# Performance work log

Measured on AMD Instinct MI355X. Metric: run time of the kernel, lower is better.

## Reference

```python
import jax, jax.numpy as jnp
import numpy as np

B, T, S, D = 8, 2048, 2048, 1024

def setup_inputs() -> dict:
    key = jax.random.key(0)
    k1, k2 = jax.random.split(key)
    trg_outs = jax.random.normal(k1, (B, T, D), dtype=jnp.float32)
    src_outs = jax.random.normal(k2, (B, S, D), dtype=jnp.float32)
    return {"trg_outs": trg_outs, "src_outs": src_outs}

def reference(trg_outs, src_outs):
    # Luong 'dot' attention: unscaled dot-product scores.
    # scores: (B, T, S)
    attn_scores = jnp.einsum('btd,bsd->bts', trg_outs, src_outs)
    attn_weights = jax.nn.softmax(attn_scores, axis=2)
    # context: (B, T, D)
    context_vec = jnp.einsum('bts,bsd->btd', attn_weights, src_outs)
    return (context_vec, attn_weights)
```

## Files before the change

### kernel.cpp

```cpp
#include <hip/hip_runtime.h>


#define BB 8
#define TT 2048
#define SS 2048
#define DD 1024

typedef float  f32x4   __attribute__((ext_vector_type(4)));
typedef float  f32x16  __attribute__((ext_vector_type(16)));
typedef short  bf16x8  __attribute__((ext_vector_type(8)));
typedef _Float16 f16x8 __attribute__((ext_vector_type(8)));
typedef _Float16 f16x4 __attribute__((ext_vector_type(4)));

static __device__ __forceinline__ unsigned short bf16_rne(float x) {
  unsigned int u = __float_as_uint(x);
  u += 0x7FFFu + ((u >> 16) & 1u);
  return (unsigned short)(u >> 16);
}

static __device__ __forceinline__ void gl2lds16(const void* g, void* l) {
  __builtin_amdgcn_global_load_lds(
      (const __attribute__((address_space(1))) unsigned int*)g,
      (__attribute__((address_space(3))) unsigned int*)l, 16, 0, 0);
}

static __device__ __forceinline__ int ldsoff_h(int r, int h) {
  return ((r >> 2) << 6) + ((((r & 3) << 1) + (h ^ ((r >> 2) & 1))) << 3);
}

__global__ __launch_bounds__(256)
void conv_trg_f16(const float* __restrict__ x, _Float16* __restrict__ h16) {
  const size_t i = ((size_t)blockIdx.x * 256 + threadIdx.x) * 8;
  float4 v0 = *(const float4*)(x + i);
  float4 v1 = *(const float4*)(x + i + 4);
  f16x8 h;
  h[0] = (_Float16)v0.x; h[1] = (_Float16)v0.y;
  h[2] = (_Float16)v0.z; h[3] = (_Float16)v0.w;
  h[4] = (_Float16)v1.x; h[5] = (_Float16)v1.y;
  h[6] = (_Float16)v1.z; h[7] = (_Float16)v1.w;
  *(f16x8*)(h16 + i) = h;
}

__global__ __launch_bounds__(256)
void conv_src_f16_hilo_t(const float* __restrict__ src,
                         _Float16* __restrict__ hi,
                         _Float16* __restrict__ lo,
                         _Float16* __restrict__ srcT) {
  const int b  = blockIdx.z;
  const int d0 = blockIdx.x * 64;
  const int s0 = blockIdx.y * 64;
  const float* S = src + (size_t)b * SS * DD;
  __shared__ _Float16 t16[64][65];
  const int t = threadIdx.x;

#pragma unroll
  for (int p = 0; p < 4; ++p) {
    const int r = p * 16 + (t >> 4);
    const int c = (t & 15) * 4;
    float4 v = *(const float4*)(S + (size_t)(s0 + r) * DD + d0 + c);
    float f[4] = {v.x, v.y, v.z, v.w};
    f16x4 h, l;
#pragma unroll
    for (int e = 0; e < 4; ++e) {
      _Float16 hv = (_Float16)f[e];
      h[e] = hv;
      l[e] = (_Float16)(f[e] - (float)hv);
      t16[r][c + e] = hv;
    }
    const size_t go = ((size_t)b * SS + s0 + r) * DD + d0 + c;
    *(f16x4*)(hi + go) = h;
    *(f16x4*)(lo + go) = l;
  }
  __syncthreads();
#pragma unroll
  for (int p = 0; p < 4; ++p) {
    const int d  = p * 16 + (t >> 4);
    const int sq = (t & 15) * 4;
    f16x4 o;
#pragma unroll
    for (int k = 0; k < 4; ++k) o[k] = t16[sq + k][d];
    *(f16x4*)(srcT + ((size_t)b * DD + d0 + d) * SS + s0 + sq) = o;
  }
}

__global__ __launch_bounds__(512, 2)
void attn_gemm1_pipe(const _Float16* __restrict__ a16,
                     const _Float16* __restrict__ bh16,
                     const _Float16* __restrict__ bl16,
                     float* __restrict__ scores) {
  const int b   = blockIdx.z;
  const int tm0 = blockIdx.y * 256;
  const int tn0 = blockIdx.x * 256;
  float* C = scores + (size_t)b * TT * SS;

  __shared__ __align__(16) _Float16 sm[3][24576];

  const int t      = threadIdx.x;
  const int lane   = t & 63;
  const int wv     = t >> 6;
  const int wm     = (wv >> 2) * 128;
  const int wn     = (wv & 3) * 64;
  const int lrow32 = lane & 31;
  const int khalf  = lane >> 5;

  const _Float16* gp[6];
  {
    const _Float16* base0 = a16  + ((size_t)b * TT + tm0) * DD;
    const _Float16* base1 = bh16 + ((size_t)b * SS + tn0) * DD;
    const _Float16* base2 = bl16 + ((size_t)b * SS + tn0) * DD;
    const _Float16* bases[3] = {base0, base1, base2};
#pragma unroll
    for (int j = 0; j < 6; ++j) {
      const int kk   = j & 1;
      const int cc   = t;
      const int line = cc >> 3, slot = cc & 7;
      const int r    = (line << 2) + (slot >> 1);
      const int h    = (slot & 1) ^ (line & 1);
      gp[j] = bases[j >> 1] + (size_t)r * DD + kk * 16 + h * 8;
    }
  }
#define STG1(buf, j) do { gl2lds16(gp[j], (buf) + ((j) * 512 + t) * 8); gp[j] += 32; } while (0)

  int aoff[4], bhoff[2], bloff[2];
#pragma unroll
  for (int mi = 0; mi < 4; ++mi)
    aoff[mi] = ldsoff_h(wm + mi * 32 + lrow32, khalf);
#pragma unroll
  for (int ni = 0; ni < 2; ++ni) {
    const int rr = wn + ni * 32 + lrow32;
    bhoff[ni] = 8192  + ldsoff_h(rr, khalf);
    bloff[ni] = 16384 + ldsoff_h(rr, khalf);
  }

  f32x16 acc[4][2];
#pragma unroll
  for (int i = 0; i < 4; ++i)
#pragma unroll
    for (int j = 0; j < 2; ++j) acc[i][j] = (f32x16)0.0f;

  _Float16* bufc = sm[0];
  _Float16* bufo = sm[1];
  _Float16* bufn = sm[2];

#pragma unroll
  for (int j = 0; j < 6; ++j) STG1(bufc, j);
#pragma unroll
  for (int j = 0; j < 6; ++j) STG1(bufo, j);
  asm volatile("s_waitcnt vmcnt(6)" ::: "memory");
  __builtin_amdgcn_s_barrier();
  __builtin_amdgcn_sched_barrier(0);

  const int NT = DD / 32;
#pragma unroll 1
  for (int tt = 0; tt < NT; ++tt) {
    const bool more = (tt + 2 < NT);

    {
      f16x8 a[4], bh[2], bl[2];
#pragma unroll
      for (int mi = 0; mi < 4; ++mi) a[mi] = *(const f16x8*)(bufc + aoff[mi]);
#pragma unroll
      for (int ni = 0; ni < 2; ++ni) {
        bh[ni] = *(const f16x8*)(bufc + bhoff[ni]);
        bl[ni] = *(const f16x8*)(bufc + bloff[ni]);
      }
      if (more) { STG1(bufn, 0); STG1(bufn, 1); STG1(bufn, 2); }
      __builtin_amdgcn_s_barrier();
      asm volatile("s_waitcnt lgkmcnt(0)" ::: "memory");
      __builtin_amdgcn_sched_barrier(0);
      __builtin_amdgcn_s_setprio(1);
#pragma unroll
      for (int mi = 0; mi < 4; ++mi)
#pragma unroll
        for (int ni = 0; ni < 2; ++ni) {
          acc[mi][ni] = __builtin_amdgcn_mfma_f32_32x32x16_f16(a[mi], bh[ni], acc[mi][ni], 0, 0, 0);
          acc[mi][ni] = __builtin_amdgcn_mfma_f32_32x32x16_f16(a[mi], bl[ni], acc[mi][ni], 0, 0, 0);
        }
      __builtin_amdgcn_s_setprio(0);
      __builtin_amdgcn_s_barrier();
      __builtin_amdgcn_sched_barrier(0);
    }

    {
      f16x8 a[4], bh[2], bl[2];
#pragma unroll
      for (int mi = 0; mi < 4; ++mi) a[mi] = *(const f16x8*)(bufc + 4096 + aoff[mi]);
#pragma unroll
      for (int ni = 0; ni < 2; ++ni) {
        bh[ni] = *(const f16x8*)(bufc + 4096 + bhoff[ni]);
        bl[ni] = *(const f16x8*)(bufc + 4096 + bloff[ni]);
      }
      if (more) { STG1(bufn, 3); STG1(bufn, 4); STG1(bufn, 5); }
      if (more) asm volatile("s_waitcnt vmcnt(6)" ::: "memory");
      else      asm volatile("s_waitcnt vmcnt(0)" ::: "memory");
      __builtin_amdgcn_s_barrier();
      asm volatile("s_waitcnt lgkmcnt(0)" ::: "memory");
      __builtin_amdgcn_sched_barrier(0);
      __builtin_amdgcn_s_setprio(1);
#pragma unroll
      for (int mi = 0; mi < 4; ++mi)
#pragma unroll
        for (int ni = 0; ni < 2; ++ni) {
          acc[mi][ni] = __builtin_amdgcn_mfma_f32_32x32x16_f16(a[mi], bh[ni], acc[mi][ni], 0, 0, 0);
          acc[mi][ni] = __builtin_amdgcn_mfma_f32_32x32x16_f16(a[mi], bl[ni], acc[mi][ni], 0, 0, 0);
        }
      __builtin_amdgcn_s_setprio(0);
      __builtin_amdgcn_s_barrier();
      __builtin_amdgcn_sched_barrier(0);
    }

    _Float16* tmp = bufc; bufc = bufo; bufo = bufn; bufn = tmp;
  }
#undef STG1

  const int rsub = 4 * khalf;
#pragma unroll
  for (int mi = 0; mi < 4; ++mi)
#pragma unroll
    for (int ni = 0; ni < 2; ++ni) {
      const int rb  = tm0 + wm + mi * 32 + rsub;
      const int col = tn0 + wn + ni * 32 + lrow32;
#pragma unroll
      for (int p = 0; p < 16; ++p)
        C[(size_t)(rb + (p & 3) + 8 * (p >> 2)) * SS + col] = acc[mi][ni][p];
    }
}

__global__ __launch_bounds__(64)
void attn_softmax_w16(float* __restrict__ w, _Float16* __restrict__ w16) {
  const size_t row = blockIdx.x;
  float4* p4 = (float4*)(w + row * SS);
  _Float16* o = w16 + row * SS;
  const int lane = threadIdx.x;

  float4 v[8];
#pragma unroll
  for (int j = 0; j < 8; ++j) v[j] = p4[lane + 64 * j];

  float m = -1e30f;
#pragma unroll
  for (int j = 0; j < 8; ++j)
    m = fmaxf(m, fmaxf(fmaxf(v[j].x, v[j].y), fmaxf(v[j].z, v[j].w)));
#pragma unroll
  for (int off = 32; off >= 1; off >>= 1) m = fmaxf(m, __shfl_xor(m, off, 64));

  float s = 0.0f;
#pragma unroll
  for (int j = 0; j < 8; ++j) {
    v[j].x = __expf(v[j].x - m); v[j].y = __expf(v[j].y - m);
    v[j].z = __expf(v[j].z - m); v[j].w = __expf(v[j].w - m);
    s += v[j].x + v[j].y + v[j].z + v[j].w;
  }
#pragma unroll
  for (int off = 32; off >= 1; off >>= 1) s += __shfl_xor(s, off, 64);

  const float inv = __fdividef(1.0f, s);
#pragma unroll
  for (int j = 0; j < 8; ++j) {
    v[j].x *= inv; v[j].y *= inv; v[j].z *= inv; v[j].w *= inv;
    p4[lane + 64 * j] = v[j];
    f16x4 h;
    h[0] = (_Float16)v[j].x; h[1] = (_Float16)v[j].y;
    h[2] = (_Float16)v[j].z; h[3] = (_Float16)v[j].w;
    *(f16x4*)(o + 4 * (lane + 64 * j)) = h;
  }
}

__global__ __launch_bounds__(512, 2)
void attn_gemm2_pipe(const _Float16* __restrict__ w16,
                     const _Float16* __restrict__ srcT,
                     float* __restrict__ out) {
  const int b   = blockIdx.z;
  const int tm0 = blockIdx.y * 256;
  const int tn0 = blockIdx.x * 256;
  float* C = out + (size_t)b * TT * DD;

  __shared__ __align__(16) _Float16 sm[3][16384];

  const int t      = threadIdx.x;
  const int lane   = t & 63;
  const int wv     = t >> 6;
  const int wm     = (wv >> 2) * 128;
  const int wn     = (wv & 3) * 64;
  const int lrow32 = lane & 31;
  const int khalf  = lane >> 5;

  const _Float16* gp[4];
  {
    const _Float16* base0 = w16  + ((size_t)b * TT + tm0) * SS;
    const _Float16* base1 = srcT + ((size_t)b * DD + tn0) * SS;
    const _Float16* bases[2] = {base0, base1};
#pragma unroll
    for (int j = 0; j < 4; ++j) {
      const int kk   = j & 1;
      const int cc   = t;
      const int line = cc >> 3, slot = cc & 7;
      const int r    = (line << 2) + (slot >> 1);
      const int h    = (slot & 1) ^ (line & 1);
      gp[j] = bases[j >> 1] + (size_t)r * SS + kk * 16 + h * 8;
    }
  }
#define STG2(buf, j) do { gl2lds16(gp[j], (buf) + ((j) * 512 + t) * 8); gp[j] += 32; } while (0)

  int aoff[4], boff[2];
#pragma unroll
  for (int mi = 0; mi < 4; ++mi)
    aoff[mi] = ldsoff_h(wm + mi * 32 + lrow32, khalf);
#pragma unroll
  for (int ni = 0; ni < 2; ++ni)
    boff[ni] = 8192 + ldsoff_h(wn + ni * 32 + lrow32, khalf);

  f32x16 acc[4][2];
#pragma unroll
  for (int i = 0; i < 4; ++i)
#pragma unroll
    for (int j = 0; j < 2; ++j) acc[i][j] = (f32x16)0.0f;

  _Float16* bufc = sm[0];
  _Float16* bufo = sm[1];
  _Float16* bufn = sm[2];

#pragma unroll
  for (int j = 0; j < 4; ++j) STG2(bufc, j);
#pragma unroll
  for (int j = 0; j < 4; ++j) STG2(bufo, j);
  asm volatile("s_waitcnt vmcnt(4)" ::: "memory");
  __builtin_amdgcn_s_barrier();
  __builtin_amdgcn_sched_barrier(0);

  const int NT = SS / 32;
#pragma unroll 1
  for (int tt = 0; tt < NT; ++tt) {
    const bool more = (tt + 2 < NT);

    {
      f16x8 a[4], bf[2];
#pragma unroll
      for (int mi = 0; mi < 4; ++mi) a[mi] = *(const f16x8*)(bufc + aoff[mi]);
#pragma unroll
      for (int ni = 0; ni < 2; ++ni) bf[ni] = *(const f16x8*)(bufc + boff[ni]);
      if (more) { STG2(bufn, 0); STG2(bufn, 2); }
      __builtin_amdgcn_s_barrier();
      asm volatile("s_waitcnt lgkmcnt(0)" ::: "memory");
      __builtin_amdgcn_sched_barrier(0);
      __builtin_amdgcn_s_setprio(1);
#pragma unroll
      for (int mi = 0; mi < 4; ++mi)
#pragma unroll
        for (int ni = 0; ni < 2; ++ni)
          acc[mi][ni] = __builtin_amdgcn_mfma_f32_32x32x16_f16(a[mi], bf[ni], acc[mi][ni], 0, 0, 0);
      __builtin_amdgcn_s_setprio(0);
      __builtin_amdgcn_s_barrier();
      __builtin_amdgcn_sched_barrier(0);
    }

    {
      f16x8 a[4], bf[2];
#pragma unroll
      for (int mi = 0; mi < 4; ++mi) a[mi] = *(const f16x8*)(bufc + 4096 + aoff[mi]);
#pragma unroll
      for (int ni = 0; ni < 2; ++ni) bf[ni] = *(const f16x8*)(bufc + 4096 + boff[ni]);
      if (more) { STG2(bufn, 1); STG2(bufn, 3); }
      if (more) asm volatile("s_waitcnt vmcnt(4)" ::: "memory");
      else      asm volatile("s_waitcnt vmcnt(0)" ::: "memory");
      __builtin_amdgcn_s_barrier();
      asm volatile("s_waitcnt lgkmcnt(0)" ::: "memory");
      __builtin_amdgcn_sched_barrier(0);
      __builtin_amdgcn_s_setprio(1);
#pragma unroll
      for (int mi = 0; mi < 4; ++mi)
#pragma unroll
        for (int ni = 0; ni < 2; ++ni)
          acc[mi][ni] = __builtin_amdgcn_mfma_f32_32x32x16_f16(a[mi], bf[ni], acc[mi][ni], 0, 0, 0);
      __builtin_amdgcn_s_setprio(0);
      __builtin_amdgcn_s_barrier();
      __builtin_amdgcn_sched_barrier(0);
    }

    _Float16* tmp = bufc; bufc = bufo; bufo = bufn; bufn = tmp;
  }
#undef STG2

  const int rsub = 4 * khalf;
#pragma unroll
  for (int mi = 0; mi < 4; ++mi)
#pragma unroll
    for (int ni = 0; ni < 2; ++ni) {
      const int rb  = tm0 + wm + mi * 32 + rsub;
      const int col = tn0 + wn + ni * 32 + lrow32;
#pragma unroll
      for (int p = 0; p < 16; ++p)
        C[(size_t)(rb + (p & 3) + 8 * (p >> 2)) * DD + col] = acc[mi][ni][p];
    }
}

__global__ __launch_bounds__(256, 1)
void attn_gemm1_scores_bf16x3(const float* __restrict__ trg,
                              const float* __restrict__ src,
                              float* __restrict__ scores) {
  const int b   = blockIdx.z;
  const int tm0 = blockIdx.y * 128;
  const int tn0 = blockIdx.x * 128;
  const float* A  = trg + (size_t)b * TT * DD;
  const float* Bm = src + (size_t)b * SS * DD;
  float* C = scores + (size_t)b * TT * SS;

  __shared__ __align__(16) unsigned short smAh[128 * 32];
  __shared__ __align__(16) unsigned short smAl[128 * 32];
  __shared__ __align__(16) unsigned short smBh[128 * 32];
  __shared__ __align__(16) unsigned short smBl[128 * 32];

  const int t     = threadIdx.x;
  const int lane  = t & 63;
  const int wv    = t >> 6;
  const int m_off = (wv & 1) * 64;
  const int n_off = (wv >> 1) * 64;
  const int q     = lane >> 4;
  const int lrow  = lane & 15;

  f32x4 acc[4][4];
#pragma unroll
  for (int i = 0; i < 4; ++i)
#pragma unroll
    for (int j = 0; j < 4; ++j) acc[i][j] = (f32x4)0.0f;

  for (int kt = 0; kt < DD; kt += 32) {
    __syncthreads();
#pragma unroll
    for (int h = 0; h < 2; ++h) {
      const int c  = t + h * 256;
      const int r  = c >> 2;
      const int j  = c & 3;
      const int gk = j ^ ((r >> 1) & 3);
      {
        const float* ga = A + (size_t)(tm0 + r) * DD + kt + gk * 8;
        float4 v0 = *(const float4*)ga;
        float4 v1 = *(const float4*)(ga + 4);
        float f[8] = {v0.x, v0.y, v0.z, v0.w, v1.x, v1.y, v1.z, v1.w};
        bf16x8 hi, lo;
#pragma unroll
        for (int e = 0; e < 8; ++e) {
          unsigned short hb = bf16_rne(f[e]);
          hi[e] = (short)hb;
          float hf = __uint_as_float(((unsigned int)hb) << 16);
          lo[e] = (short)bf16_rne(f[e] - hf);
        }
        *(bf16x8*)(smAh + c * 8) = hi;
        *(bf16x8*)(smAl + c * 8) = lo;
      }
      {
        const float* gb = Bm + (size_t)(tn0 + r) * DD + kt + gk * 8;
        float4 v0 = *(const float4*)gb;
        float4 v1 = *(const float4*)(gb + 4);
        float f[8] = {v0.x, v0.y, v0.z, v0.w, v1.x, v1.y, v1.z, v1.w};
        bf16x8 hi, lo;
#pragma unroll
        for (int e = 0; e < 8; ++e) {
          unsigned short hb = bf16_rne(f[e]);
          hi[e] = (short)hb;
          float hf = __uint_as_float(((unsigned int)hb) << 16);
          lo[e] = (short)bf16_rne(f[e] - hf);
        }
        *(bf16x8*)(smBh + c * 8) = hi;
        *(bf16x8*)(smBl + c * 8) = lo;
      }
    }
    __syncthreads();

    bf16x8 ah[4], al[4], bh[4], bl[4];
#pragma unroll
    for (int mi = 0; mi < 4; ++mi) {
      const int r   = m_off + mi * 16 + lrow;
      const int off = (r * 4 + (q ^ ((r >> 1) & 3))) * 8;
      ah[mi] = *(const bf16x8*)(smAh + off);
      al[mi] = *(const bf16x8*)(smAl + off);
    }
#pragma unroll
    for (int ni = 0; ni < 4; ++ni) {
      const int r   = n_off + ni * 16 + lrow;
      const int off = (r * 4 + (q ^ ((r >> 1) & 3))) * 8;
      bh[ni] = *(const bf16x8*)(smBh + off);
      bl[ni] = *(const bf16x8*)(smBl + off);
    }
#pragma unroll
    for (int mi = 0; mi < 4; ++mi)
#pragma unroll
      for (int ni = 0; ni < 4; ++ni) {
        acc[mi][ni] = __builtin_amdgcn_mfma_f32_16x16x32_bf16(al[mi], bh[ni], acc[mi][ni], 0, 0, 0);
        acc[mi][ni] = __builtin_amdgcn_mfma_f32_16x16x32_bf16(ah[mi], bl[ni], acc[mi][ni], 0, 0, 0);
        acc[mi][ni] = __builtin_amdgcn_mfma_f32_16x16x32_bf16(ah[mi], bh[ni], acc[mi][ni], 0, 0, 0);
      }
  }

#pragma unroll
  for (int mi = 0; mi < 4; ++mi)
#pragma unroll
    for (int ni = 0; ni < 4; ++ni) {
      const int row0 = tm0 + m_off + mi * 16 + q * 4;
      const int col  = tn0 + n_off + ni * 16 + lrow;
#pragma unroll
      for (int p = 0; p < 4; ++p)
        C[(size_t)(row0 + p) * SS + col] = acc[mi][ni][p];
    }
}

__global__ __launch_bounds__(256)
void attn_softmax_rows(float* __restrict__ w) {
  float* p = w + (size_t)blockIdx.x * SS;
  const int t = threadIdx.x;
  float4* p4 = (float4*)p;
  float4 v0 = p4[t];
  float4 v1 = p4[t + 256];

  float m = fmaxf(fmaxf(fmaxf(v0.x, v0.y), fmaxf(v0.z, v0.w)),
                  fmaxf(fmaxf(v1.x, v1.y), fmaxf(v1.z, v1.w)));
#pragma unroll
  for (int off = 32; off >= 1; off >>= 1) m = fmaxf(m, __shfl_xor(m, off, 64));
  __shared__ float redm[4];
  __shared__ float reds[4];
  const int wv = t >> 6, lane = t & 63;
  if (lane == 0) redm[wv] = m;
  __syncthreads();
  m = fmaxf(fmaxf(redm[0], redm[1]), fmaxf(redm[2], redm[3]));

  v0.x = __expf(v0.x - m); v0.y = __expf(v0.y - m);
  v0.z = __expf(v0.z - m); v0.w = __expf(v0.w - m);
  v1.x = __expf(v1.x - m); v1.y = __expf(v1.y - m);
  v1.z = __expf(v1.z - m); v1.w = __expf(v1.w - m);

  float s = v0.x + v0.y + v0.z + v0.w + v1.x + v1.y + v1.z + v1.w;
#pragma unroll
  for (int off = 32; off >= 1; off >>= 1) s += __shfl_xor(s, off, 64);
  if (lane == 0) reds[wv] = s;
  __syncthreads();
  s = reds[0] + reds[1] + reds[2] + reds[3];

  const float inv = __fdividef(1.0f, s);
  v0.x *= inv; v0.y *= inv; v0.z *= inv; v0.w *= inv;
  v1.x *= inv; v1.y *= inv; v1.z *= inv; v1.w *= inv;
  p4[t] = v0;
  p4[t + 256] = v1;
}

__global__ __launch_bounds__(256, 1)
void attn_gemm2_ctx_f16(const float* __restrict__ w,
                        const float* __restrict__ src,
                        float* __restrict__ out) {
  const int b   = blockIdx.z;
  const int tm0 = blockIdx.y * 128;
  const int tn0 = blockIdx.x * 128;
  const float* A  = w + (size_t)b * TT * SS;
  const float* Bs = src + (size_t)b * SS * DD;
  float* C = out + (size_t)b * TT * DD;

  __shared__ __align__(16) _Float16 smA[128 * 32];
  __shared__ __align__(16) _Float16 smB[128 * 32];

  const int t     = threadIdx.x;
  const int lane  = t & 63;
  const int wv    = t >> 6;
  const int m_off = (wv & 1) * 64;
  const int n_off = (wv >> 1) * 64;
  const int q     = lane >> 4;
  const int lrow  = lane & 15;

  const int bn    = t & 127;
  const int bh2   = t >> 7;
  const int bs2   = (bn >> 1) & 3;
  const int slot0 = (2 * bh2) ^ bs2;
  const int slot1 = (2 * bh2 + 1) ^ bs2;

  f32x4 acc[4][4];
#pragma unroll
  for (int i = 0; i < 4; ++i)
#pragma unroll
    for (int j = 0; j < 4; ++j) acc[i][j] = (f32x4)0.0f;

  for (int kt = 0; kt < SS; kt += 32) {
    __syncthreads();
#pragma unroll
    for (int h = 0; h < 2; ++h) {
      const int c  = t + h * 256;
      const int r  = c >> 2;
      const int j  = c & 3;
      const int gk = j ^ ((r >> 1) & 3);
      const float* ga = A + (size_t)(tm0 + r) * SS + kt + gk * 8;
      float4 v0 = *(const float4*)ga;
      float4 v1 = *(const float4*)(ga + 4);
      f16x8 hv;
      hv[0] = (_Float16)v0.x; hv[1] = (_Float16)v0.y;
      hv[2] = (_Float16)v0.z; hv[3] = (_Float16)v0.w;
      hv[4] = (_Float16)v1.x; hv[5] = (_Float16)v1.y;
      hv[6] = (_Float16)v1.z; hv[7] = (_Float16)v1.w;
      *(f16x8*)(smA + c * 8) = hv;
    }
    {
      const float* gb = Bs + (size_t)(kt + bh2 * 16) * DD + (tn0 + bn);
      f16x8 c0, c1;
#pragma unroll
      for (int kk = 0; kk < 8; ++kk) c0[kk] = (_Float16)gb[(size_t)kk * DD];
#pragma unroll
      for (int kk = 0; kk < 8; ++kk) c1[kk] = (_Float16)gb[(size_t)(kk + 8) * DD];
      *(f16x8*)(smB + bn * 32 + slot0 * 8) = c0;
      *(f16x8*)(smB + bn * 32 + slot1 * 8) = c1;
    }
    __syncthreads();

    f16x8 af[4], bfr[4];
#pragma unroll
    for (int mi = 0; mi < 4; ++mi) {
      const int r   = m_off + mi * 16 + lrow;
      const int off = (r * 4 + (q ^ ((r >> 1) & 3))) * 8;
      af[mi] = *(const f16x8*)(smA + off);
    }
#pragma unroll
    for (int ni = 0; ni < 4; ++ni) {
      const int n   = n_off + ni * 16 + lrow;
      const int off = n * 32 + (q ^ ((n >> 1) & 3)) * 8;
      bfr[ni] = *(const f16x8*)(smB + off);
    }
#pragma unroll
    for (int mi = 0; mi < 4; ++mi)
#pragma unroll
      for (int ni = 0; ni < 4; ++ni)
        acc[mi][ni] = __builtin_amdgcn_mfma_f32_16x16x32_f16(af[mi], bfr[ni], acc[mi][ni], 0, 0, 0);
  }

#pragma unroll
  for (int mi = 0; mi < 4; ++mi)
#pragma unroll
    for (int ni = 0; ni < 4; ++ni) {
      const int row0 = tm0 + m_off + mi * 16 + q * 4;
      const int col  = tn0 + n_off + ni * 16 + lrow;
#pragma unroll
      for (int p = 0; p < 4; ++p)
        C[(size_t)(row0 + p) * DD + col] = acc[mi][ni][p];
    }
}

extern "C" void kernel_launch(void* const* d_in, const int* in_sizes, int n_in,
                              void* d_out, int out_size, void* d_ws, size_t ws_size,
                              hipStream_t stream) {
  const float* trg = (const float*)d_in[0];
  const float* src = (const float*)d_in[1];
  float* ctx = (float*)d_out;
  float* wts = (float*)d_out + (size_t)BB * TT * DD;

  const size_t NT = (size_t)BB * TT * DD;
  const size_t NW = (size_t)BB * TT * SS;
  const size_t need = (4 * NT + NW) * 2;

  if (ws_size >= need) {
    _Float16* tH16 = (_Float16*)d_ws;
    _Float16* sH16 = tH16 + NT;
    _Float16* sL16 = sH16 + NT;
    _Float16* srcT = sL16 + NT;
    _Float16* w16  = srcT + NT;

    conv_trg_f16<<<dim3(NT / (8 * 256)), 256, 0, stream>>>(trg, tH16);
    conv_src_f16_hilo_t<<<dim3(DD / 64, SS / 64, BB), 256, 0, stream>>>(src, sH16, sL16, srcT);
    attn_gemm1_pipe<<<dim3(SS / 256, TT / 256, BB), 512, 0, stream>>>(tH16, sH16, sL16, wts);
    attn_softmax_w16<<<dim3(BB * TT), 64, 0, stream>>>(wts, w16);
    attn_gemm2_pipe<<<dim3(DD / 256, TT / 256, BB), 512, 0, stream>>>(w16, srcT, ctx);
  } else {
    attn_gemm1_scores_bf16x3<<<dim3(SS / 128, TT / 128, BB), 256, 0, stream>>>(trg, src, wts);
    attn_softmax_rows<<<dim3(BB * TT), 256, 0, stream>>>(wts);
    attn_gemm2_ctx_f16<<<dim3(DD / 128, TT / 128, BB), 256, 0, stream>>>(wts, src, ctx);
  }
}
```

Before: 575.5 us.

## Fuse fp32-to-fp16 weight conversion into second GEMM, drop fp16 weight buffer

The softmax kernel no longer writes a separate fp16 copy of the attention weights. The second GEMM now loads fp32 weights into registers, converts them to fp16 and stores them into LDS, while srcT is still staged directly into LDS. This removes a 64MB fp16 write and re-read, but the GEMM now reads fp32 weights (twice the bytes) once per DD/256 column block. It also replaces the 3-buffer direct-to-LDS pipeline with 2-buffer software prefetch through registers, which adds register pressure.

```diff
diff --git a/kernel.cpp b/kernel.cpp
--- a/kernel.cpp
+++ b/kernel.cpp
@@ -227,10 +227,9 @@
 }
 
 __global__ __launch_bounds__(64)
-void attn_softmax_w16(float* __restrict__ w, _Float16* __restrict__ w16) {
+void attn_softmax_inplace(float* __restrict__ w) {
   const size_t row = blockIdx.x;
   float4* p4 = (float4*)(w + row * SS);
-  _Float16* o = w16 + row * SS;
   const int lane = threadIdx.x;
 
   float4 v[8];
@@ -259,23 +258,21 @@
   for (int j = 0; j < 8; ++j) {
     v[j].x *= inv; v[j].y *= inv; v[j].z *= inv; v[j].w *= inv;
     p4[lane + 64 * j] = v[j];
-    f16x4 h;
-    h[0] = (_Float16)v[j].x; h[1] = (_Float16)v[j].y;
-    h[2] = (_Float16)v[j].z; h[3] = (_Float16)v[j].w;
-    *(f16x4*)(o + 4 * (lane + 64 * j)) = h;
   }
 }
 
 __global__ __launch_bounds__(512, 2)
-void attn_gemm2_pipe(const _Float16* __restrict__ w16,
-                     const _Float16* __restrict__ srcT,
-                     float* __restrict__ out) {
+void attn_g2_fused(const float* __restrict__ w,
+                   const _Float16* __restrict__ srcT,
+                   float* __restrict__ out) {
   const int b   = blockIdx.z;
+  const int tn0 = blockIdx.x * 256;
   const int tm0 = blockIdx.y * 256;
-  const int tn0 = blockIdx.x * 256;
+  const float* W = w + (size_t)b * TT * SS;
   float* C = out + (size_t)b * TT * DD;
 
-  __shared__ __align__(16) _Float16 sm[3][16384];
+  __shared__ __align__(16) _Float16 smA[2][8192];
+  __shared__ __align__(16) _Float16 smB[2][8192];
 
   const int t      = threadIdx.x;
   const int lane   = t & 63;
@@ -285,22 +282,24 @@
   const int lrow32 = lane & 31;
   const int khalf  = lane >> 5;
 
-  const _Float16* gp[4];
-  {
-    const _Float16* base0 = w16  + ((size_t)b * TT + tm0) * SS;
-    const _Float16* base1 = srcT + ((size_t)b * DD + tn0) * SS;
-    const _Float16* bases[2] = {base0, base1};
-#pragma unroll
-    for (int j = 0; j < 4; ++j) {
-      const int kk   = j & 1;
-      const int cc   = t;
-      const int line = cc >> 3, slot = cc & 7;
-      const int r    = (line << 2) + (slot >> 1);
-      const int h    = (slot & 1) ^ (line & 1);
-      gp[j] = bases[j >> 1] + (size_t)r * SS + kk * 16 + h * 8;
-    }
-  }
-#define STG2(buf, j) do { gl2lds16(gp[j], (buf) + ((j) * 512 + t) * 8); gp[j] += 32; } while (0)
+  const float* gw[4];
+  int wadr[4];
+#pragma unroll
+  for (int p = 0; p < 4; ++p) {
+    const int c    = p * 512 + t;
+    const int rloc = c >> 3;
+    const int f4   = c & 7;
+    const int kk   = f4 >> 2;
+    const int h    = (f4 >> 1) & 1;
+    const int sub  = f4 & 1;
+    wadr[p] = kk * 4096 + ldsoff_h(rloc, h) + sub * 4;
+    gw[p] = W + (size_t)(tm0 + rloc) * SS + f4 * 4;
+  }
+
+  const int ar = (t >> 3) * 4 + ((t & 7) >> 1);
+  const int ah = ((t & 7) & 1) ^ ((t >> 3) & 1);
+  const _Float16* gpB0 = srcT + ((size_t)b * DD + tn0 + ar) * SS + ah * 8;
+  const _Float16* gpB1 = gpB0 + 16;
 
   int aoff[4], boff[2];
 #pragma unroll
@@ -308,7 +307,7 @@
     aoff[mi] = ldsoff_h(wm + mi * 32 + lrow32, khalf);
 #pragma unroll
   for (int ni = 0; ni < 2; ++ni)
-    boff[ni] = 8192 + ldsoff_h(wn + ni * 32 + lrow32, khalf);
+    boff[ni] = ldsoff_h(wn + ni * 32 + lrow32, khalf);
 
   f32x16 acc[4][2];
 #pragma unroll
@@ -316,70 +315,105 @@
 #pragma unroll
     for (int j = 0; j < 2; ++j) acc[i][j] = (f32x16)0.0f;
 
-  _Float16* bufc = sm[0];
-  _Float16* bufo = sm[1];
-  _Float16* bufn = sm[2];
-
-#pragma unroll
-  for (int j = 0; j < 4; ++j) STG2(bufc, j);
-#pragma unroll
-  for (int j = 0; j < 4; ++j) STG2(bufo, j);
+  float4 wvA[4], wvB[4];
+
+  _Float16* Ac = smA[0];
+  _Float16* An = smA[1];
+  _Float16* Bc = smB[0];
+  _Float16* Bn = smB[1];
+
+#define G2F_LOADW(S)                                   \
+  do {                                                 \
+    S[0] = *(const float4*)gw[0]; gw[0] += 32;         \
+    S[1] = *(const float4*)gw[1]; gw[1] += 32;         \
+    S[2] = *(const float4*)gw[2]; gw[2] += 32;         \
+    S[3] = *(const float4*)gw[3]; gw[3] += 32;         \
+  } while (0)
+
+#define G2F_CVT(S, DST)                                                     \
+  do {                                                                      \
+    _Pragma("unroll") for (int p = 0; p < 4; ++p) {                         \
+      f16x4 hh;                                                             \
+      hh[0] = (_Float16)S[p].x; hh[1] = (_Float16)S[p].y;                   \
+      hh[2] = (_Float16)S[p].z; hh[3] = (_Float16)S[p].w;                   \
+      *(f16x4*)((DST) + wadr[p]) = hh;                                      \
+    }                                                                       \
+  } while (0)
+
+#define G2F_STAGEB(DST)                                \
+  do {                                                 \
+    gl2lds16(gpB0, (DST) + t * 8);                     \
+    gl2lds16(gpB1, (DST) + 4096 + t * 8);              \
+    gpB0 += 32; gpB1 += 32;                            \
+  } while (0)
+
+#define G2F_MFMA_READS(A0, B0, A1, B1)                                      \
+  f16x8 A0[4], B0[2], A1[4], B1[2];                                         \
+  _Pragma("unroll") for (int mi = 0; mi < 4; ++mi)                          \
+    A0[mi] = *(const f16x8*)(Ac + aoff[mi]);                                \
+  _Pragma("unroll") for (int ni = 0; ni < 2; ++ni)                          \
+    B0[ni] = *(const f16x8*)(Bc + boff[ni]);                                \
+  _Pragma("unroll") for (int mi = 0; mi < 4; ++mi)                          \
+    A1[mi] = *(const f16x8*)(Ac + 4096 + aoff[mi]);                         \
+  _Pragma("unroll") for (int ni = 0; ni < 2; ++ni)                          \
+    B1[ni] = *(const f16x8*)(Bc + 4096 + boff[ni]);
+
+#define G2F_MFMA16(A0, B0, A1, B1)                                          \
+  __builtin_amdgcn_s_setprio(1);                                            \
+  _Pragma("unroll") for (int mi = 0; mi < 4; ++mi)                          \
+    _Pragma("unroll") for (int ni = 0; ni < 2; ++ni)                        \
+      acc[mi][ni] = __builtin_amdgcn_mfma_f32_32x32x16_f16(A0[mi], B0[ni], acc[mi][ni], 0, 0, 0); \
+  _Pragma("unroll") for (int mi = 0; mi < 4; ++mi)                          \
+    _Pragma("unroll") for (int ni = 0; ni < 2; ++ni)                        \
+      acc[mi][ni] = __builtin_amdgcn_mfma_f32_32x32x16_f16(A1[mi], B1[ni], acc[mi][ni], 0, 0, 0); \
+  __builtin_amdgcn_s_setprio(0);
+
+#define G2F_ITER(WC, WL, DOB, DOW, VME)                                     \
+  {                                                                         \
+    if (DOB) G2F_STAGEB(Bn);                                                \
+    G2F_MFMA_READS(a0, b0, a1, b1)                                          \
+    asm volatile("s_waitcnt vmcnt(2)" ::: "memory");                        \
+    G2F_CVT(WC, An);                                                        \
+    if (DOW) G2F_LOADW(WL);                                                 \
+    asm volatile("s_waitcnt lgkmcnt(0)" ::: "memory");                      \
+    __builtin_amdgcn_sched_barrier(0);                                      \
+    G2F_MFMA16(a0, b0, a1, b1)                                              \
+    asm volatile("s_waitcnt vmcnt(" #VME ")" ::: "memory");                 \
+    __builtin_amdgcn_s_barrier();                                           \
+    __builtin_amdgcn_sched_barrier(0);                                      \
+    _Float16* tA = Ac; Ac = An; An = tA;                                    \
+    _Float16* tB = Bc; Bc = Bn; Bn = tB;                                    \
+  }
+
+  G2F_LOADW(wvA);
+  G2F_STAGEB(Bc);
+  asm volatile("s_waitcnt vmcnt(2)" ::: "memory");
+  G2F_CVT(wvA, Ac);
+  G2F_LOADW(wvA);
   asm volatile("s_waitcnt vmcnt(4)" ::: "memory");
+  asm volatile("s_waitcnt lgkmcnt(0)" ::: "memory");
   __builtin_amdgcn_s_barrier();
   __builtin_amdgcn_sched_barrier(0);
 
-  const int NT = SS / 32;
 #pragma unroll 1
-  for (int tt = 0; tt < NT; ++tt) {
-    const bool more = (tt + 2 < NT);
-
-    {
-      f16x8 a[4], bf[2];
-#pragma unroll
-      for (int mi = 0; mi < 4; ++mi) a[mi] = *(const f16x8*)(bufc + aoff[mi]);
-#pragma unroll
-      for (int ni = 0; ni < 2; ++ni) bf[ni] = *(const f16x8*)(bufc + boff[ni]);
-      if (more) { STG2(bufn, 0); STG2(bufn, 2); }
-      __builtin_amdgcn_s_barrier();
-      asm volatile("s_waitcnt lgkmcnt(0)" ::: "memory");
-      __builtin_amdgcn_sched_barrier(0);
-      __builtin_amdgcn_s_setprio(1);
-#pragma unroll
-      for (int mi = 0; mi < 4; ++mi)
-#pragma unroll
-        for (int ni = 0; ni < 2; ++ni)
-          acc[mi][ni] = __builtin_amdgcn_mfma_f32_32x32x16_f16(a[mi], bf[ni], acc[mi][ni], 0, 0, 0);
-      __builtin_amdgcn_s_setprio(0);
-      __builtin_amdgcn_s_barrier();
-      __builtin_amdgcn_sched_barrier(0);
-    }
-
-    {
-      f16x8 a[4], bf[2];
-#pragma unroll
-      for (int mi = 0; mi < 4; ++mi) a[mi] = *(const f16x8*)(bufc + 4096 + aoff[mi]);
-#pragma unroll
-      for (int ni = 0; ni < 2; ++ni) bf[ni] = *(const f16x8*)(bufc + 4096 + boff[ni]);
-      if (more) { STG2(bufn, 1); STG2(bufn, 3); }
-      if (more) asm volatile("s_waitcnt vmcnt(4)" ::: "memory");
-      else      asm volatile("s_waitcnt vmcnt(0)" ::: "memory");
-      __builtin_amdgcn_s_barrier();
-      asm volatile("s_waitcnt lgkmcnt(0)" ::: "memory");
-      __builtin_amdgcn_sched_barrier(0);
-      __builtin_amdgcn_s_setprio(1);
-#pragma unroll
-      for (int mi = 0; mi < 4; ++mi)
-#pragma unroll
-        for (int ni = 0; ni < 2; ++ni)
-          acc[mi][ni] = __builtin_amdgcn_mfma_f32_32x32x16_f16(a[mi], bf[ni], acc[mi][ni], 0, 0, 0);
-      __builtin_amdgcn_s_setprio(0);
-      __builtin_amdgcn_s_barrier();
-      __builtin_amdgcn_sched_barrier(0);
-    }
-
-    _Float16* tmp = bufc; bufc = bufo; bufo = bufn; bufn = tmp;
-  }
-#undef STG2
+  for (int it = 0; it < 31; ++it) {
+    G2F_ITER(wvA, wvB, 1, 1, 4);
+    G2F_ITER(wvB, wvA, 1, 1, 4);
+  }
+  G2F_ITER(wvA, wvB, 1, 0, 0);
+  {
+    G2F_MFMA_READS(a0, b0, a1, b1)
+    asm volatile("s_waitcnt lgkmcnt(0)" ::: "memory");
+    __builtin_amdgcn_sched_barrier(0);
+    G2F_MFMA16(a0, b0, a1, b1)
+  }
+
+#undef G2F_ITER
+#undef G2F_MFMA16
+#undef G2F_MFMA_READS
+#undef G2F_STAGEB
+#undef G2F_CVT
+#undef G2F_LOADW
 
   const int rsub = 4 * khalf;
 #pragma unroll
@@ -647,21 +681,19 @@
   float* wts = (float*)d_out + (size_t)BB * TT * DD;
 
   const size_t NT = (size_t)BB * TT * DD;
-  const size_t NW = (size_t)BB * TT * SS;
-  const size_t need = (4 * NT + NW) * 2;
+  const size_t need = 4 * NT * 2;
 
   if (ws_size >= need) {
     _Float16* tH16 = (_Float16*)d_ws;
     _Float16* sH16 = tH16 + NT;
     _Float16* sL16 = sH16 + NT;
     _Float16* srcT = sL16 + NT;
-    _Float16* w16  = srcT + NT;
 
     conv_trg_f16<<<dim3(NT / (8 * 256)), 256, 0, stream>>>(trg, tH16);
     conv_src_f16_hilo_t<<<dim3(DD / 64, SS / 64, BB), 256, 0, stream>>>(src, sH16, sL16, srcT);
     attn_gemm1_pipe<<<dim3(SS / 256, TT / 256, BB), 512, 0, stream>>>(tH16, sH16, sL16, wts);
-    attn_softmax_w16<<<dim3(BB * TT), 64, 0, stream>>>(wts, w16);
-    attn_gemm2_pipe<<<dim3(DD / 256, TT / 256, BB), 512, 0, stream>>>(w16, srcT, ctx);
+    attn_softmax_inplace<<<dim3(BB * TT), 64, 0, stream>>>(wts);
+    attn_g2_fused<<<dim3(DD / 256, TT / 256, BB), 512, 0, stream>>>(wts, srcT, ctx);
   } else {
     attn_gemm1_scores_bf16x3<<<dim3(SS / 128, TT / 128, BB), 256, 0, stream>>>(trg, src, wts);
     attn_softmax_rows<<<dim3(BB * TT), 256, 0, stream>>>(wts);
```

Measured after the change: 569.7 us. No clear change (-1.0%).

## Shrink gemm2 M-tile to 128, merge k-halves per barrier, pack softmax rows

Applied to the files above, without the earlier changes.

The context GEMM now uses 128x256 tiles instead of 256x256, which doubles the block count (256 to 512 blocks) for better CU fill and lowers per-thread accumulator registers. The pipeline issues all three LDS stage loads for a k-step at once and processes both 16-wide k-halves before a single barrier, replacing the four barriers per iteration. The softmax kernel packs four rows per 256-thread block instead of one row per 64-thread block, cutting the block count. The costs are more total global traffic for the srcT operand, since each B tile is reloaded by twice as many blocks, and less reuse of each B fragment.

```diff
diff --git a/kernel.cpp b/kernel.cpp
--- a/kernel.cpp
+++ b/kernel.cpp
@@ -226,12 +226,12 @@
     }
 }
 
-__global__ __launch_bounds__(64)
+__global__ __launch_bounds__(256)
 void attn_softmax_w16(float* __restrict__ w, _Float16* __restrict__ w16) {
-  const size_t row = blockIdx.x;
+  const size_t row = (size_t)blockIdx.x * 4 + (threadIdx.x >> 6);
+  const int lane = threadIdx.x & 63;
   float4* p4 = (float4*)(w + row * SS);
   _Float16* o = w16 + row * SS;
-  const int lane = threadIdx.x;
 
   float4 v[8];
 #pragma unroll
@@ -271,48 +271,54 @@
                      const _Float16* __restrict__ srcT,
                      float* __restrict__ out) {
   const int b   = blockIdx.z;
-  const int tm0 = blockIdx.y * 256;
+  const int tm0 = blockIdx.y * 128;
   const int tn0 = blockIdx.x * 256;
   float* C = out + (size_t)b * TT * DD;
 
-  __shared__ __align__(16) _Float16 sm[3][16384];
+  __shared__ __align__(16) _Float16 sm[3][12288];
 
   const int t      = threadIdx.x;
   const int lane   = t & 63;
   const int wv     = t >> 6;
-  const int wm     = (wv >> 2) * 128;
+  const int wm     = (wv >> 2) * 64;
   const int wn     = (wv & 3) * 64;
   const int lrow32 = lane & 31;
   const int khalf  = lane >> 5;
 
-  const _Float16* gp[4];
-  {
-    const _Float16* base0 = w16  + ((size_t)b * TT + tm0) * SS;
-    const _Float16* base1 = srcT + ((size_t)b * DD + tn0) * SS;
-    const _Float16* bases[2] = {base0, base1};
-#pragma unroll
-    for (int j = 0; j < 4; ++j) {
-      const int kk   = j & 1;
-      const int cc   = t;
-      const int line = cc >> 3, slot = cc & 7;
-      const int r    = (line << 2) + (slot >> 1);
-      const int h    = (slot & 1) ^ (line & 1);
-      gp[j] = bases[j >> 1] + (size_t)r * SS + kk * 16 + h * 8;
-    }
-  }
-#define STG2(buf, j) do { gl2lds16(gp[j], (buf) + ((j) * 512 + t) * 8); gp[j] += 32; } while (0)
-
-  int aoff[4], boff[2];
-#pragma unroll
-  for (int mi = 0; mi < 4; ++mi)
+  const int ccA = t & 255, kkA = t >> 8;
+  const int slA = ccA & 7, lnA = ccA >> 3;
+  const int rA  = lnA * 4 + (slA >> 1);
+  const int hA  = (slA & 1) ^ (lnA & 1);
+  const _Float16* gpA = w16 + ((size_t)b * TT + tm0 + rA) * SS + kkA * 16 + hA * 8;
+  const int dstA = kkA * 2048 + ccA * 8;
+
+  const int slB = t & 7, lnB = t >> 3;
+  const int rB  = lnB * 4 + (slB >> 1);
+  const int hB  = (slB & 1) ^ (lnB & 1);
+  const _Float16* gpB0 = srcT + ((size_t)b * DD + tn0 + rB) * SS + hB * 8;
+  const _Float16* gpB1 = gpB0 + 16;
+  const int dstB0 = 4096 + t * 8;
+  const int dstB1 = 8192 + t * 8;
+
+#define STG2(buf)                                      \
+  do {                                                 \
+    gl2lds16(gpA,  (buf) + dstA);                      \
+    gl2lds16(gpB0, (buf) + dstB0);                     \
+    gl2lds16(gpB1, (buf) + dstB1);                     \
+    gpA += 32; gpB0 += 32; gpB1 += 32;                 \
+  } while (0)
+
+  int aoff[2], boff[2];
+#pragma unroll
+  for (int mi = 0; mi < 2; ++mi)
     aoff[mi] = ldsoff_h(wm + mi * 32 + lrow32, khalf);
 #pragma unroll
   for (int ni = 0; ni < 2; ++ni)
-    boff[ni] = 8192 + ldsoff_h(wn + ni * 32 + lrow32, khalf);
-
-  f32x16 acc[4][2];
-#pragma unroll
-  for (int i = 0; i < 4; ++i)
+    boff[ni] = ldsoff_h(wn + ni * 32 + lrow32, khalf);
+
+  f32x16 acc[2][2];
+#pragma unroll
+  for (int i = 0; i < 2; ++i)
 #pragma unroll
     for (int j = 0; j < 2; ++j) acc[i][j] = (f32x16)0.0f;
 
@@ -320,11 +326,9 @@
   _Float16* bufo = sm[1];
   _Float16* bufn = sm[2];
 
-#pragma unroll
-  for (int j = 0; j < 4; ++j) STG2(bufc, j);
-#pragma unroll
-  for (int j = 0; j < 4; ++j) STG2(bufo, j);
-  asm volatile("s_waitcnt vmcnt(4)" ::: "memory");
+  STG2(bufc);
+  STG2(bufo);
+  asm volatile("s_waitcnt vmcnt(3)" ::: "memory");
   __builtin_amdgcn_s_barrier();
   __builtin_amdgcn_sched_barrier(0);
 
@@ -332,50 +336,30 @@
 #pragma unroll 1
   for (int tt = 0; tt < NT; ++tt) {
     const bool more = (tt + 2 < NT);
-
-    {
-      f16x8 a[4], bf[2];
-#pragma unroll
-      for (int mi = 0; mi < 4; ++mi) a[mi] = *(const f16x8*)(bufc + aoff[mi]);
-#pragma unroll
-      for (int ni = 0; ni < 2; ++ni) bf[ni] = *(const f16x8*)(bufc + boff[ni]);
-      if (more) { STG2(bufn, 0); STG2(bufn, 2); }
-      __builtin_amdgcn_s_barrier();
-      asm volatile("s_waitcnt lgkmcnt(0)" ::: "memory");
-      __builtin_amdgcn_sched_barrier(0);
+    if (more) STG2(bufn);
+
+#pragma unroll
+    for (int kk = 0; kk < 2; ++kk) {
+      f16x8 a[2], bf[2];
+#pragma unroll
+      for (int mi = 0; mi < 2; ++mi)
+        a[mi] = *(const f16x8*)(bufc + kk * 2048 + aoff[mi]);
+#pragma unroll
+      for (int ni = 0; ni < 2; ++ni)
+        bf[ni] = *(const f16x8*)(bufc + 4096 + kk * 4096 + boff[ni]);
       __builtin_amdgcn_s_setprio(1);
 #pragma unroll
-      for (int mi = 0; mi < 4; ++mi)
+      for (int mi = 0; mi < 2; ++mi)
 #pragma unroll
         for (int ni = 0; ni < 2; ++ni)
           acc[mi][ni] = __builtin_amdgcn_mfma_f32_32x32x16_f16(a[mi], bf[ni], acc[mi][ni], 0, 0, 0);
       __builtin_amdgcn_s_setprio(0);
-      __builtin_amdgcn_s_barrier();
-      __builtin_amdgcn_sched_barrier(0);
-    }
-
-    {
-      f16x8 a[4], bf[2];
-#pragma unroll
-      for (int mi = 0; mi < 4; ++mi) a[mi] = *(const f16x8*)(bufc + 4096 + aoff[mi]);
-#pragma unroll
-      for (int ni = 0; ni < 2; ++ni) bf[ni] = *(const f16x8*)(bufc + 4096 + boff[ni]);
-      if (more) { STG2(bufn, 1); STG2(bufn, 3); }
-      if (more) asm volatile("s_waitcnt vmcnt(4)" ::: "memory");
-      else      asm volatile("s_waitcnt vmcnt(0)" ::: "memory");
-      __builtin_amdgcn_s_barrier();
-      asm volatile("s_waitcnt lgkmcnt(0)" ::: "memory");
-      __builtin_amdgcn_sched_barrier(0);
-      __builtin_amdgcn_s_setprio(1);
-#pragma unroll
-      for (int mi = 0; mi < 4; ++mi)
-#pragma unroll
-        for (int ni = 0; ni < 2; ++ni)
-          acc[mi][ni] = __builtin_amdgcn_mfma_f32_32x32x16_f16(a[mi], bf[ni], acc[mi][ni], 0, 0, 0);
-      __builtin_amdgcn_s_setprio(0);
-      __builtin_amdgcn_s_barrier();
-      __builtin_amdgcn_sched_barrier(0);
-    }
+    }
+
+    if (more) asm volatile("s_waitcnt vmcnt(3)" ::: "memory");
+    else      asm volatile("s_waitcnt vmcnt(0)" ::: "memory");
+    __builtin_amdgcn_s_barrier();
+    __builtin_amdgcn_sched_barrier(0);
 
     _Float16* tmp = bufc; bufc = bufo; bufo = bufn; bufn = tmp;
   }
@@ -383,7 +367,7 @@
 
   const int rsub = 4 * khalf;
 #pragma unroll
-  for (int mi = 0; mi < 4; ++mi)
+  for (int mi = 0; mi < 2; ++mi)
 #pragma unroll
     for (int ni = 0; ni < 2; ++ni) {
       const int rb  = tm0 + wm + mi * 32 + rsub;
@@ -660,8 +644,8 @@
     conv_trg_f16<<<dim3(NT / (8 * 256)), 256, 0, stream>>>(trg, tH16);
     conv_src_f16_hilo_t<<<dim3(DD / 64, SS / 64, BB), 256, 0, stream>>>(src, sH16, sL16, srcT);
     attn_gemm1_pipe<<<dim3(SS / 256, TT / 256, BB), 512, 0, stream>>>(tH16, sH16, sL16, wts);
-    attn_softmax_w16<<<dim3(BB * TT), 64, 0, stream>>>(wts, w16);
-    attn_gemm2_pipe<<<dim3(DD / 256, TT / 256, BB), 512, 0, stream>>>(w16, srcT, ctx);
+    attn_softmax_w16<<<dim3(BB * TT / 4), 256, 0, stream>>>(wts, w16);
+    attn_gemm2_pipe<<<dim3(DD / 256, TT / 128, BB), 512, 0, stream>>>(w16, srcT, ctx);
   } else {
     attn_gemm1_scores_bf16x3<<<dim3(SS / 128, TT / 128, BB), 256, 0, stream>>>(trg, src, wts);
     attn_softmax_rows<<<dim3(BB * TT), 256, 0, stream>>>(wts);
```

After: 573.4 us. Within noise of the previous version (-0.4%).

## Software-pipeline LDS fragment reads against MFMA and cut barriers per k-tile

Applied to the files above, without the earlier changes.

Restructures the main loops of both fp16 GEMM kernels so the second half-tile's LDS fragments load while the first half's MFMAs run. The first half-tile of the next k-tile is prefetched into registers right after the barrier. All global-to-LDS stages for the next buffer are issued at once, and the loop drops from four barriers per k-tile to one. This is meant to hide LDS latency and barrier stalls behind matrix math, at the cost of more live vector registers. It relies on hand-chosen lgkmcnt values, which could be wrong if the compiler emits a different number of LDS instructions.

```diff
diff --git a/kernel.cpp b/kernel.cpp
--- a/kernel.cpp
+++ b/kernel.cpp
@@ -134,13 +134,49 @@
 
   f32x16 acc[4][2];
 #pragma unroll
+  for (int i = 0; i < 2; ++i) {}
+#pragma unroll
   for (int i = 0; i < 4; ++i)
 #pragma unroll
     for (int j = 0; j < 2; ++j) acc[i][j] = (f32x16)0.0f;
+
+  f16x8 a0[4], bh0[2], bl0[2];
+  f16x8 a1[4], bh1[2], bl1[2];
 
   _Float16* bufc = sm[0];
   _Float16* bufo = sm[1];
   _Float16* bufn = sm[2];
+
+#define G1_READ_P0()                                                        \
+  do {                                                                      \
+    _Pragma("unroll") for (int mi = 0; mi < 4; ++mi)                        \
+      a0[mi] = *(const f16x8*)(bufc + aoff[mi]);                            \
+    _Pragma("unroll") for (int ni = 0; ni < 2; ++ni) {                      \
+      bh0[ni] = *(const f16x8*)(bufc + bhoff[ni]);                          \
+      bl0[ni] = *(const f16x8*)(bufc + bloff[ni]);                          \
+    }                                                                       \
+  } while (0)
+
+#define G1_READ_P1()                                                        \
+  do {                                                                      \
+    _Pragma("unroll") for (int mi = 0; mi < 4; ++mi)                        \
+      a1[mi] = *(const f16x8*)(bufc + 4096 + aoff[mi]);                     \
+    _Pragma("unroll") for (int ni = 0; ni < 2; ++ni) {                      \
+      bh1[ni] = *(const f16x8*)(bufc + 4096 + bhoff[ni]);                   \
+      bl1[ni] = *(const f16x8*)(bufc + 4096 + bloff[ni]);                   \
+    }                                                                       \
+  } while (0)
+
+#define G1_MFMA(AA, BH, BL)                                                 \
+  do {                                                                      \
+    __builtin_amdgcn_s_setprio(1);                                          \
+    _Pragma("unroll") for (int mi = 0; mi < 4; ++mi)                        \
+      _Pragma("unroll") for (int ni = 0; ni < 2; ++ni) {                    \
+        acc[mi][ni] = __builtin_amdgcn_mfma_f32_32x32x16_f16(AA[mi], BH[ni], acc[mi][ni], 0, 0, 0); \
+        acc[mi][ni] = __builtin_amdgcn_mfma_f32_32x32x16_f16(AA[mi], BL[ni], acc[mi][ni], 0, 0, 0); \
+      }                                                                     \
+    __builtin_amdgcn_s_setprio(0);                                          \
+  } while (0)
 
 #pragma unroll
   for (int j = 0; j < 6; ++j) STG1(bufc, j);
@@ -149,68 +185,38 @@
   asm volatile("s_waitcnt vmcnt(6)" ::: "memory");
   __builtin_amdgcn_s_barrier();
   __builtin_amdgcn_sched_barrier(0);
+  G1_READ_P0();
+  __builtin_amdgcn_sched_barrier(0);
 
   const int NT = DD / 32;
 #pragma unroll 1
   for (int tt = 0; tt < NT; ++tt) {
     const bool more = (tt + 2 < NT);
 
-    {
-      f16x8 a[4], bh[2], bl[2];
-#pragma unroll
-      for (int mi = 0; mi < 4; ++mi) a[mi] = *(const f16x8*)(bufc + aoff[mi]);
-#pragma unroll
-      for (int ni = 0; ni < 2; ++ni) {
-        bh[ni] = *(const f16x8*)(bufc + bhoff[ni]);
-        bl[ni] = *(const f16x8*)(bufc + bloff[ni]);
-      }
-      if (more) { STG1(bufn, 0); STG1(bufn, 1); STG1(bufn, 2); }
-      __builtin_amdgcn_s_barrier();
-      asm volatile("s_waitcnt lgkmcnt(0)" ::: "memory");
+    if (more) { STG1(bufn, 0); STG1(bufn, 1); STG1(bufn, 2);
+                STG1(bufn, 3); STG1(bufn, 4); STG1(bufn, 5); }
+    G1_READ_P1();
+    asm volatile("s_waitcnt lgkmcnt(8)" ::: "memory");
+    __builtin_amdgcn_sched_barrier(0);
+    G1_MFMA(a0, bh0, bl0);
+    asm volatile("s_waitcnt lgkmcnt(0)" ::: "memory");
+    __builtin_amdgcn_sched_barrier(0);
+    G1_MFMA(a1, bh1, bl1);
+
+    if (more) asm volatile("s_waitcnt vmcnt(6)" ::: "memory");
+    else      asm volatile("s_waitcnt vmcnt(0)" ::: "memory");
+    __builtin_amdgcn_s_barrier();
+    __builtin_amdgcn_sched_barrier(0);
+
+    _Float16* tmp = bufc; bufc = bufo; bufo = bufn; bufn = tmp;
+    if (tt + 1 < NT) {
+      G1_READ_P0();
       __builtin_amdgcn_sched_barrier(0);
-      __builtin_amdgcn_s_setprio(1);
-#pragma unroll
-      for (int mi = 0; mi < 4; ++mi)
-#pragma unroll
-        for (int ni = 0; ni < 2; ++ni) {
-          acc[mi][ni] = __builtin_amdgcn_mfma_f32_32x32x16_f16(a[mi], bh[ni], acc[mi][ni], 0, 0, 0);
-          acc[mi][ni] = __builtin_amdgcn_mfma_f32_32x32x16_f16(a[mi], bl[ni], acc[mi][ni], 0, 0, 0);
-        }
-      __builtin_amdgcn_s_setprio(0);
-      __builtin_amdgcn_s_barrier();
-      __builtin_amdgcn_sched_barrier(0);
-    }
-
-    {
-      f16x8 a[4], bh[2], bl[2];
-#pragma unroll
-      for (int mi = 0; mi < 4; ++mi) a[mi] = *(const f16x8*)(bufc + 4096 + aoff[mi]);
-#pragma unroll
-      for (int ni = 0; ni < 2; ++ni) {
-        bh[ni] = *(const f16x8*)(bufc + 4096 + bhoff[ni]);
-        bl[ni] = *(const f16x8*)(bufc + 4096 + bloff[ni]);
-      }
-      if (more) { STG1(bufn, 3); STG1(bufn, 4); STG1(bufn, 5); }
-      if (more) asm volatile("s_waitcnt vmcnt(6)" ::: "memory");
-      else      asm volatile("s_waitcnt vmcnt(0)" ::: "memory");
-      __builtin_amdgcn_s_barrier();
-      asm volatile("s_waitcnt lgkmcnt(0)" ::: "memory");
-      __builtin_amdgcn_sched_barrier(0);
-      __builtin_amdgcn_s_setprio(1);
-#pragma unroll
-      for (int mi = 0; mi < 4; ++mi)
-#pragma unroll
-        for (int ni = 0; ni < 2; ++ni) {
-          acc[mi][ni] = __builtin_amdgcn_mfma_f32_32x32x16_f16(a[mi], bh[ni], acc[mi][ni], 0, 0, 0);
-          acc[mi][ni] = __builtin_amdgcn_mfma_f32_32x32x16_f16(a[mi], bl[ni], acc[mi][ni], 0, 0, 0);
-        }
-      __builtin_amdgcn_s_setprio(0);
-      __builtin_amdgcn_s_barrier();
-      __builtin_amdgcn_sched_barrier(0);
-    }
-
-    _Float16* tmp = bufc; bufc = bufo; bufo = bufn; bufn = tmp;
-  }
+    }
+  }
+#undef G1_MFMA
+#undef G1_READ_P1
+#undef G1_READ_P0
 #undef STG1
 
   const int rsub = 4 * khalf;
@@ -316,9 +322,37 @@
 #pragma unroll
     for (int j = 0; j < 2; ++j) acc[i][j] = (f32x16)0.0f;
 
+  f16x8 a0[4], b0[2];
+  f16x8 a1[4], b1[2];
+
   _Float16* bufc = sm[0];
   _Float16* bufo = sm[1];
   _Float16* bufn = sm[2];
+
+#define G2_READ_P0()                                                        \
+  do {                                                                      \
+    _Pragma("unroll") for (int mi = 0; mi < 4; ++mi)                        \
+      a0[mi] = *(const f16x8*)(bufc + aoff[mi]);                            \
+    _Pragma("unroll") for (int ni = 0; ni < 2; ++ni)                        \
+      b0[ni] = *(const f16x8*)(bufc + boff[ni]);                            \
+  } while (0)
+
+#define G2_READ_P1()                                                        \
+  do {                                                                      \
+    _Pragma("unroll") for (int mi = 0; mi < 4; ++mi)                        \
+      a1[mi] = *(const f16x8*)(bufc + 4096 + aoff[mi]);                     \
+    _Pragma("unroll") for (int ni = 0; ni < 2; ++ni)                        \
+      b1[ni] = *(const f16x8*)(bufc + 4096 + boff[ni]);                     \
+  } while (0)
+
+#define G2_MFMA(AA, BF)                                                     \
+  do {                                                                      \
+    __builtin_amdgcn_s_setprio(1);                                          \
+    _Pragma("unroll") for (int mi = 0; mi < 4; ++mi)                        \
+      _Pragma("unroll") for (int ni = 0; ni < 2; ++ni)                      \
+        acc[mi][ni] = __builtin_amdgcn_mfma_f32_32x32x16_f16(AA[mi], BF[ni], acc[mi][ni], 0, 0, 0); \
+    __builtin_amdgcn_s_setprio(0);                                          \
+  } while (0)
 
 #pragma unroll
   for (int j = 0; j < 4; ++j) STG2(bufc, j);
@@ -327,58 +361,37 @@
   asm volatile("s_waitcnt vmcnt(4)" ::: "memory");
   __builtin_amdgcn_s_barrier();
   __builtin_amdgcn_sched_barrier(0);
+  G2_READ_P0();
+  __builtin_amdgcn_sched_barrier(0);
 
   const int NT = SS / 32;
 #pragma unroll 1
   for (int tt = 0; tt < NT; ++tt) {
     const bool more = (tt + 2 < NT);
 
-    {
-      f16x8 a[4], bf[2];
-#pragma unroll
-      for (int mi = 0; mi < 4; ++mi) a[mi] = *(const f16x8*)(bufc + aoff[mi]);
-#pragma unroll
-      for (int ni = 0; ni < 2; ++ni) bf[ni] = *(const f16x8*)(bufc + boff[ni]);
-      if (more) { STG2(bufn, 0); STG2(bufn, 2); }
-      __builtin_amdgcn_s_barrier();
-      asm volatile("s_waitcnt lgkmcnt(0)" ::: "memory");
+    if (more) { STG2(bufn, 0); STG2(bufn, 1); STG2(bufn, 2); STG2(bufn, 3); }
+    G2_READ_P1();
+    asm volatile("s_waitcnt lgkmcnt(6)" ::: "memory");
+    __builtin_amdgcn_sched_barrier(0);
+    G2_MFMA(a0, b0);
+    asm volatile("s_waitcnt lgkmcnt(0)" ::: "memory");
+    __builtin_amdgcn_sched_barrier(0);
+    G2_MFMA(a1, b1);
+
+    if (more) asm volatile("s_waitcnt vmcnt(4)" ::: "memory");
+    else      asm volatile("s_waitcnt vmcnt(0)" ::: "memory");
+    __builtin_amdgcn_s_barrier();
+    __builtin_amdgcn_sched_barrier(0);
+
+    _Float16* tmp = bufc; bufc = bufo; bufo = bufn; bufn = tmp;
+    if (tt + 1 < NT) {
+      G2_READ_P0();
       __builtin_amdgcn_sched_barrier(0);
-      __builtin_amdgcn_s_setprio(1);
-#pragma unroll
-      for (int mi = 0; mi < 4; ++mi)
-#pragma unroll
-        for (int ni = 0; ni < 2; ++ni)
-          acc[mi][ni] = __builtin_amdgcn_mfma_f32_32x32x16_f16(a[mi], bf[ni], acc[mi][ni], 0, 0, 0);
-      __builtin_amdgcn_s_setprio(0);
-      __builtin_amdgcn_s_barrier();
-      __builtin_amdgcn_sched_barrier(0);
-    }
-
-    {
-      f16x8 a[4], bf[2];
-#pragma unroll
-      for (int mi = 0; mi < 4; ++mi) a[mi] = *(const f16x8*)(bufc + 4096 + aoff[mi]);
-#pragma unroll
-      for (int ni = 0; ni < 2; ++ni) bf[ni] = *(const f16x8*)(bufc + 4096 + boff[ni]);
-      if (more) { STG2(bufn, 1); STG2(bufn, 3); }
-      if (more) asm volatile("s_waitcnt vmcnt(4)" ::: "memory");
-      else      asm volatile("s_waitcnt vmcnt(0)" ::: "memory");
-      __builtin_amdgcn_s_barrier();
-      asm volatile("s_waitcnt lgkmcnt(0)" ::: "memory");
-      __builtin_amdgcn_sched_barrier(0);
-      __builtin_amdgcn_s_setprio(1);
-#pragma unroll
-      for (int mi = 0; mi < 4; ++mi)
-#pragma unroll
-        for (int ni = 0; ni < 2; ++ni)
-          acc[mi][ni] = __builtin_amdgcn_mfma_f32_32x32x16_f16(a[mi], bf[ni], acc[mi][ni], 0, 0, 0);
-      __builtin_amdgcn_s_setprio(0);
-      __builtin_amdgcn_s_barrier();
-      __builtin_amdgcn_sched_barrier(0);
-    }
-
-    _Float16* tmp = bufc; bufc = bufo; bufo = bufn; bufn = tmp;
-  }
+    }
+  }
+#undef G2_MFMA
+#undef G2_READ_P1
+#undef G2_READ_P0
 #undef STG2
 
   const int rsub = 4 * khalf;
```

Measured after the change: 557.9 us. 3.1% less time.
